# Kernel tuning notes

Hardware: AMD Instinct MI355X
Metric: run time of the kernel (lower is better)

## Reference

```python
import jax, jax.numpy as jnp
import numpy as np

B, LQ, LK, H, A = 32, 2048, 2048, 1024, 512


def setup_inputs() -> dict:
    key = jax.random.key(0)
    ks = jax.random.split(key, 5)
    s = 1.0 / np.sqrt(H)
    return {
        "query": jax.random.normal(ks[0], (B, LQ, H), jnp.float32),
        "key": jax.random.normal(ks[1], (B, LK, H), jnp.float32),
        "Wq": jax.random.normal(ks[2], (H, A), jnp.float32) * s,
        "bq": jnp.zeros((A,), jnp.float32),
        "Wk": jax.random.normal(ks[3], (H, A), jnp.float32) * s,
        "bk": jnp.zeros((A,), jnp.float32),
        "Wv": jax.random.normal(ks[4], (A, 1), jnp.float32) * (1.0 / np.sqrt(A)),
        "bv": jnp.zeros((1,), jnp.float32),
    }


def reference(query, key, Wq, bq, Wk, bk, Wv, bv):
    # Linear projections
    Qp = jnp.einsum("bqh,ha->bqa", query, Wq) + bq          # [B, LQ, A]
    Kp = jnp.einsum("bkh,ha->bka", key, Wk) + bk            # [B, LK, A]
    # Score matrix Q(query) @ K(key)^T
    alpha_mat = jnp.einsum("bqa,bka->bqk", Qp, Kp)          # [B, LQ, LK]
    # Sum over query dim, softmax over key dim
    alpha = jax.nn.softmax(alpha_mat.sum(axis=1, keepdims=True), axis=2)  # [B, 1, LK]
    # Per-key scalar head V applied to projected keys, then weighted combine
    v = jnp.einsum("bka,ao->bko", Kp, Wv) + bv              # [B, LK, 1]
    x = jnp.matmul(alpha, v)[:, 0, :]                        # [B, 1]
    return x
```

## Files before the change

kernel.cpp:

```cpp
#include <hip/hip_runtime.h>
#include <math.h>

#define NB 32
#define LQ 2048
#define LK 2048
#define HD 1024
#define AD 512
#define QCH 32

__global__ void __launch_bounds__(256) k1_qreduce(const float* __restrict__ query,
                                                 const float* __restrict__ Wk,
                                                 const float* __restrict__ Wv,
                                                 const float* __restrict__ bk,
                                                 const float* __restrict__ bv,
                                                 float* __restrict__ partial,
                                                 float* __restrict__ wv_eff,
                                                 float* __restrict__ c_v) {
    int bid = blockIdx.x;
    if (bid < NB * QCH) {
        int b = bid / QCH, qc = bid % QCH;
        int t = threadIdx.x;
        const int QPC = LQ / QCH;
        float4 a0 = {0.f, 0.f, 0.f, 0.f};
        float4 a1 = {0.f, 0.f, 0.f, 0.f};
        const float4* src = (const float4*)(query + ((size_t)b * LQ + (size_t)qc * QPC) * HD);
        for (int q = 0; q < QPC; q += 2) {
            float4 v0 = src[(size_t)q * (HD / 4) + t];
            float4 v1 = src[(size_t)(q + 1) * (HD / 4) + t];
            a0.x += v0.x; a0.y += v0.y; a0.z += v0.z; a0.w += v0.w;
            a1.x += v1.x; a1.y += v1.y; a1.z += v1.z; a1.w += v1.w;
        }
        float4 acc = {a0.x + a1.x, a0.y + a1.y, a0.z + a1.z, a0.w + a1.w};
        float4* dst = (float4*)(partial + ((size_t)qc * NB + b) * HD);
        dst[t] = acc;
    } else if (bid < NB * QCH + 16) {
        int w = threadIdx.x >> 6, lane = threadIdx.x & 63;
        int gw = (bid - NB * QCH) * 4 + w;
        const float4* vv = (const float4*)(Wv);
        for (int r = 0; r < 16; ++r) {
            int h = gw * 16 + r;
            const float4* wr = (const float4*)(Wk + (size_t)h * AD);
            double acc = 0.0;
            #pragma unroll
            for (int j = 0; j < 2; ++j) {
                int f = lane + 64 * j;
                float4 w4 = wr[f];
                float4 v4 = vv[f];
                acc += (double)w4.x * (double)v4.x + (double)w4.y * (double)v4.y
                     + (double)w4.z * (double)v4.z + (double)w4.w * (double)v4.w;
            }
            #pragma unroll
            for (int off = 32; off > 0; off >>= 1) acc += __shfl_down(acc, off);
            if (lane == 0) wv_eff[h] = (float)acc;
        }
    } else {
        if (threadIdx.x < 64) {
            int lane = threadIdx.x;
            const float4* br = (const float4*)(bk);
            const float4* vv = (const float4*)(Wv);
            double acc = 0.0;
            #pragma unroll
            for (int j = 0; j < 2; ++j) {
                int f = lane + 64 * j;
                float4 b4 = br[f];
                float4 v4 = vv[f];
                acc += (double)b4.x * (double)v4.x + (double)b4.y * (double)v4.y
                     + (double)b4.z * (double)v4.z + (double)b4.w * (double)v4.w;
            }
            #pragma unroll
            for (int off = 32; off > 0; off >>= 1) acc += __shfl_down(acc, off);
            if (lane == 0) c_v[0] = (float)(acc + (double)bv[0]);
        }
    }
}

__global__ void __launch_bounds__(256) kB_qsum(const float* __restrict__ partial,
                                               const float* __restrict__ Wq,
                                               const float* __restrict__ bq,
                                               float* __restrict__ qsum) {
    __shared__ float sq[HD];
    __shared__ double red[4][64];
    int b = blockIdx.x >> 3;
    int a0 = (blockIdx.x & 7) * 64;
    int t = threadIdx.x;

    #pragma unroll
    for (int c = 0; c < 4; ++c) {
        int h = t + c * 256;
        float acc = 0.f;
        #pragma unroll 4
        for (int qc = 0; qc < QCH; ++qc)
            acc += partial[((size_t)qc * NB + b) * HD + h];
        sq[h] = acc;
    }
    __syncthreads();

    int w = t >> 6, lane = t & 63;
    int a = a0 + lane;
    const float* wp = Wq + a;
    double c0 = 0.0, c1 = 0.0, c2 = 0.0, c3 = 0.0;
    int hbase = w * 256;
    for (int i = 0; i < 256; i += 4) {
        int h = hbase + i;
        c0 += (double)sq[h]     * (double)wp[(size_t)h * AD];
        c1 += (double)sq[h + 1] * (double)wp[(size_t)(h + 1) * AD];
        c2 += (double)sq[h + 2] * (double)wp[(size_t)(h + 2) * AD];
        c3 += (double)sq[h + 3] * (double)wp[(size_t)(h + 3) * AD];
    }
    red[w][lane] = ((c0 + c1) + (c2 + c3));
    __syncthreads();
    if (t < 64) {
        double s = red[0][t] + red[1][t] + red[2][t] + red[3][t];
        qsum[(size_t)b * AD + a0 + t] = (float)(s + (double)LQ * (double)bq[a0 + t]);
    }
}

__global__ void __launch_bounds__(256) k4_weff(const float* __restrict__ qsum,
                                               const float* __restrict__ Wk,
                                               float* __restrict__ wk_eff) {
    int w = threadIdx.x >> 6, lane = threadIdx.x & 63;
    int widx = blockIdx.x * 4 + w;
    int b = widx >> 10, h = widx & (HD - 1);
    const float4* wr = (const float4*)(Wk + (size_t)h * AD);
    const float4* qs = (const float4*)(qsum + (size_t)b * AD);
    double acc = 0.0;
    #pragma unroll
    for (int j = 0; j < 2; ++j) {
        int f = lane + 64 * j;
        float4 w4 = wr[f];
        float4 q4 = qs[f];
        acc += (double)w4.x * (double)q4.x + (double)w4.y * (double)q4.y
             + (double)w4.z * (double)q4.z + (double)w4.w * (double)q4.w;
    }
    #pragma unroll
    for (int off = 32; off > 0; off >>= 1) acc += __shfl_down(acc, off);
    if (lane == 0) wk_eff[widx] = (float)acc;
}

__global__ void __launch_bounds__(256) k5_scores(const float* __restrict__ key,
                                                 const float* __restrict__ wk_eff,
                                                 const float* __restrict__ wv_eff,
                                                 const float* __restrict__ c_v,
                                                 float* __restrict__ scores,
                                                 float* __restrict__ vvals) {
    __shared__ float lwk[HD];
    __shared__ float lwv[HD];
    int bid = blockIdx.x;
    int b = bid >> 6;
    int k0 = (bid & 63) * 32;
    for (int i = threadIdx.x; i < HD; i += 256) {
        lwk[i] = wk_eff[(size_t)b * HD + i];
        lwv[i] = wv_eff[i];
    }
    __syncthreads();
    int w = threadIdx.x >> 6;
    int lane = threadIdx.x & 63;
    double cv = (double)c_v[0];
    const float4* lwk4 = (const float4*)lwk;
    const float4* lwv4 = (const float4*)lwv;
    for (int r = 0; r < 8; ++r) {
        int k = k0 + w * 8 + r;
        const float4* kr = (const float4*)(key + ((size_t)b * LK + k) * HD);
        double sc = 0.0, vv = 0.0;
        #pragma unroll
        for (int j = 0; j < 4; ++j) {
            int f = lane + 64 * j;
            float4 kv  = kr[f];
            float4 wk4 = lwk4[f];
            float4 wv4 = lwv4[f];
            sc += (double)kv.x * (double)wk4.x + (double)kv.y * (double)wk4.y
                + (double)kv.z * (double)wk4.z + (double)kv.w * (double)wk4.w;
            vv += (double)kv.x * (double)wv4.x + (double)kv.y * (double)wv4.y
                + (double)kv.z * (double)wv4.z + (double)kv.w * (double)wv4.w;
        }
        #pragma unroll
        for (int off = 32; off > 0; off >>= 1) {
            sc += __shfl_down(sc, off);
            vv += __shfl_down(vv, off);
        }
        if (lane == 0) {
            scores[(size_t)b * LK + k] = (float)sc;
            vvals[(size_t)b * LK + k]  = (float)(vv + cv);
        }
    }
}

__global__ void __launch_bounds__(256) k6_softmax(const float* __restrict__ scores,
                                                  const float* __restrict__ vvals,
                                                  float* __restrict__ out) {
    int b = blockIdx.x;
    int t = threadIdx.x;
    __shared__ float smax_sh[4];
    __shared__ double num_sh[4], den_sh[4];
    const float* sr = scores + (size_t)b * LK;
    const float* vr = vvals  + (size_t)b * LK;
    float m = -INFINITY;
    for (int k = t; k < LK; k += 256) m = fmaxf(m, sr[k]);
    #pragma unroll
    for (int off = 32; off > 0; off >>= 1) m = fmaxf(m, __shfl_down(m, off));
    int w = t >> 6, lane = t & 63;
    if (lane == 0) smax_sh[w] = m;
    __syncthreads();
    float gm = fmaxf(fmaxf(smax_sh[0], smax_sh[1]), fmaxf(smax_sh[2], smax_sh[3]));
    double num = 0.0, den = 0.0;
    for (int k = t; k < LK; k += 256) {
        double e = exp((double)(sr[k] - gm));
        den += e;
        num += e * (double)vr[k];
    }
    #pragma unroll
    for (int off = 32; off > 0; off >>= 1) {
        num += __shfl_down(num, off);
        den += __shfl_down(den, off);
    }
    if (lane == 0) { num_sh[w] = num; den_sh[w] = den; }
    __syncthreads();
    if (t == 0) {
        double N = num_sh[0] + num_sh[1] + num_sh[2] + num_sh[3];
        double D = den_sh[0] + den_sh[1] + den_sh[2] + den_sh[3];
        out[b] = (float)(N / D);
    }
}

extern "C" void kernel_launch(void* const* d_in, const int* in_sizes, int n_in,
                              void* d_out, int out_size, void* d_ws, size_t ws_size,
                              hipStream_t stream) {
    const float* query = (const float*)d_in[0];
    const float* key   = (const float*)d_in[1];
    const float* Wq    = (const float*)d_in[2];
    const float* bq    = (const float*)d_in[3];
    const float* Wk    = (const float*)d_in[4];
    const float* bk    = (const float*)d_in[5];
    const float* Wv    = (const float*)d_in[6];
    const float* bv    = (const float*)d_in[7];
    float* out = (float*)d_out;

    float* ws = (float*)d_ws;
    size_t off = 0;
    float* partial = ws + off; off += (size_t)QCH * NB * HD;
    float* qsum    = ws + off; off += (size_t)NB * AD;
    float* wk_eff  = ws + off; off += (size_t)NB * HD;
    float* wv_eff  = ws + off; off += (size_t)HD;
    float* c_v     = ws + off; off += 1;
    float* scores  = ws + off; off += (size_t)NB * LK;
    float* vvals   = ws + off; off += (size_t)NB * LK;

    hipLaunchKernelGGL(k1_qreduce, dim3(NB * QCH + 16 + 1), dim3(256), 0, stream,
                       query, Wk, Wv, bk, bv, partial, wv_eff, c_v);
    hipLaunchKernelGGL(kB_qsum, dim3(NB * 8), dim3(256), 0, stream, partial, Wq, bq, qsum);
    hipLaunchKernelGGL(k4_weff, dim3(NB * HD / 4), dim3(256), 0, stream, qsum, Wk, wk_eff);
    hipLaunchKernelGGL(k5_scores, dim3(NB * (LK / 32)), dim3(256), 0, stream,
                       key, wk_eff, wv_eff, c_v, scores, vvals);
    hipLaunchKernelGGL(k6_softmax, dim3(NB), dim3(256), 0, stream, scores, vvals, out);
}
```

Baseline: 148.6 us.

## Fuse query projection and key-weight reduction into one per-batch kernel

Merges the qsum projection kernel and the effective key-weight kernel into one kernel, launched as a single 512-thread block per batch, so the intermediate qsum no longer goes through global memory and one launch disappears. Also doubles the number of query chunks in the streaming reduction and unrolls it four-wide, and makes the score kernel process two key rows per pass to expose more loads in flight. The price is that the fused stage runs on only 32 blocks. Each block streams all of Wq and Wk serially with double-precision accumulation, which may leave most of the GPU idle.

```diff
diff --git a/kernel.cpp b/kernel.cpp
--- a/kernel.cpp
+++ b/kernel.cpp
@@ -6,37 +6,38 @@
 #define LK 2048
 #define HD 1024
 #define AD 512
-#define QCH 32
-
-__global__ void __launch_bounds__(256) k1_qreduce(const float* __restrict__ query,
-                                                 const float* __restrict__ Wk,
-                                                 const float* __restrict__ Wv,
-                                                 const float* __restrict__ bk,
-                                                 const float* __restrict__ bv,
-                                                 float* __restrict__ partial,
-                                                 float* __restrict__ wv_eff,
-                                                 float* __restrict__ c_v) {
-    int bid = blockIdx.x;
+#define QCH 64
+
+__global__ void __launch_bounds__(256)
+k1_stream(const float* __restrict__ query, const float* __restrict__ Wk,
+          const float* __restrict__ Wv, const float* __restrict__ bk,
+          const float* __restrict__ bv, float* __restrict__ partial,
+          float* __restrict__ wv_eff, float* __restrict__ c_v) {
+    const int bid = blockIdx.x;
+    const int t = threadIdx.x;
     if (bid < NB * QCH) {
         int b = bid / QCH, qc = bid % QCH;
-        int t = threadIdx.x;
         const int QPC = LQ / QCH;
-        float4 a0 = {0.f, 0.f, 0.f, 0.f};
-        float4 a1 = {0.f, 0.f, 0.f, 0.f};
+        float4 a0 = {0.f,0.f,0.f,0.f}, a1 = {0.f,0.f,0.f,0.f};
+        float4 a2 = {0.f,0.f,0.f,0.f}, a3 = {0.f,0.f,0.f,0.f};
         const float4* src = (const float4*)(query + ((size_t)b * LQ + (size_t)qc * QPC) * HD);
-        for (int q = 0; q < QPC; q += 2) {
-            float4 v0 = src[(size_t)q * (HD / 4) + t];
+        for (int q = 0; q < QPC; q += 4) {
+            float4 v0 = src[(size_t)(q + 0) * (HD / 4) + t];
             float4 v1 = src[(size_t)(q + 1) * (HD / 4) + t];
+            float4 v2 = src[(size_t)(q + 2) * (HD / 4) + t];
+            float4 v3 = src[(size_t)(q + 3) * (HD / 4) + t];
             a0.x += v0.x; a0.y += v0.y; a0.z += v0.z; a0.w += v0.w;
             a1.x += v1.x; a1.y += v1.y; a1.z += v1.z; a1.w += v1.w;
-        }
-        float4 acc = {a0.x + a1.x, a0.y + a1.y, a0.z + a1.z, a0.w + a1.w};
-        float4* dst = (float4*)(partial + ((size_t)qc * NB + b) * HD);
-        dst[t] = acc;
+            a2.x += v2.x; a2.y += v2.y; a2.z += v2.z; a2.w += v2.w;
+            a3.x += v3.x; a3.y += v3.y; a3.z += v3.z; a3.w += v3.w;
+        }
+        float4 acc = {(a0.x + a1.x) + (a2.x + a3.x), (a0.y + a1.y) + (a2.y + a3.y),
+                      (a0.z + a1.z) + (a2.z + a3.z), (a0.w + a1.w) + (a2.w + a3.w)};
+        ((float4*)(partial + ((size_t)qc * NB + b) * HD))[t] = acc;
     } else if (bid < NB * QCH + 16) {
-        int w = threadIdx.x >> 6, lane = threadIdx.x & 63;
+        int w = t >> 6, lane = t & 63;
         int gw = (bid - NB * QCH) * 4 + w;
-        const float4* vv = (const float4*)(Wv);
+        const float4* vv = (const float4*)Wv;
         for (int r = 0; r < 16; ++r) {
             int h = gw * 16 + r;
             const float4* wr = (const float4*)(Wk + (size_t)h * AD);
@@ -46,148 +47,154 @@
                 int f = lane + 64 * j;
                 float4 w4 = wr[f];
                 float4 v4 = vv[f];
-                acc += (double)w4.x * (double)v4.x + (double)w4.y * (double)v4.y
-                     + (double)w4.z * (double)v4.z + (double)w4.w * (double)v4.w;
+                acc += (double)w4.x * v4.x + (double)w4.y * v4.y
+                     + (double)w4.z * v4.z + (double)w4.w * v4.w;
             }
             #pragma unroll
             for (int off = 32; off > 0; off >>= 1) acc += __shfl_down(acc, off);
             if (lane == 0) wv_eff[h] = (float)acc;
         }
-    } else {
-        if (threadIdx.x < 64) {
-            int lane = threadIdx.x;
-            const float4* br = (const float4*)(bk);
-            const float4* vv = (const float4*)(Wv);
-            double acc = 0.0;
-            #pragma unroll
-            for (int j = 0; j < 2; ++j) {
-                int f = lane + 64 * j;
-                float4 b4 = br[f];
-                float4 v4 = vv[f];
-                acc += (double)b4.x * (double)v4.x + (double)b4.y * (double)v4.y
-                     + (double)b4.z * (double)v4.z + (double)b4.w * (double)v4.w;
-            }
-            #pragma unroll
-            for (int off = 32; off > 0; off >>= 1) acc += __shfl_down(acc, off);
-            if (lane == 0) c_v[0] = (float)(acc + (double)bv[0]);
-        }
-    }
-}
-
-__global__ void __launch_bounds__(256) kB_qsum(const float* __restrict__ partial,
-                                               const float* __restrict__ Wq,
-                                               const float* __restrict__ bq,
-                                               float* __restrict__ qsum) {
+    } else if (t < 64) {
+        int lane = t;
+        const float4* br = (const float4*)bk;
+        const float4* vv = (const float4*)Wv;
+        double acc = 0.0;
+        #pragma unroll
+        for (int j = 0; j < 2; ++j) {
+            int f = lane + 64 * j;
+            float4 b4 = br[f];
+            float4 v4 = vv[f];
+            acc += (double)b4.x * v4.x + (double)b4.y * v4.y
+                 + (double)b4.z * v4.z + (double)b4.w * v4.w;
+        }
+        #pragma unroll
+        for (int off = 32; off > 0; off >>= 1) acc += __shfl_down(acc, off);
+        if (lane == 0) c_v[0] = (float)(acc + (double)bv[0]);
+    }
+}
+
+__global__ void __launch_bounds__(512)
+k2_qk(const float* __restrict__ partial, const float* __restrict__ Wq,
+      const float* __restrict__ bq, const float* __restrict__ Wk,
+      float* __restrict__ wk_eff) {
     __shared__ float sq[HD];
-    __shared__ double red[4][64];
-    int b = blockIdx.x >> 3;
-    int a0 = (blockIdx.x & 7) * 64;
-    int t = threadIdx.x;
-
-    #pragma unroll
-    for (int c = 0; c < 4; ++c) {
-        int h = t + c * 256;
-        float acc = 0.f;
-        #pragma unroll 4
-        for (int qc = 0; qc < QCH; ++qc)
-            acc += partial[((size_t)qc * NB + b) * HD + h];
-        sq[h] = acc;
+    __shared__ float qs[AD];
+    const int b = blockIdx.x;
+    const int t = threadIdx.x;
+
+    {
+        float ax = 0.f, ay = 0.f;
+        for (int qc = 0; qc < QCH; ++qc) {
+            const float* p = partial + ((size_t)qc * NB + b) * HD + 2 * t;
+            ax += p[0];
+            ay += p[1];
+        }
+        sq[2 * t] = ax;
+        sq[2 * t + 1] = ay;
+    }
+    __syncthreads();
+
+    {
+        int a = t;
+        const float* wp = Wq + a;
+        double c0 = 0.0, c1 = 0.0;
+        for (int h = 0; h < HD; h += 2) {
+            c0 += (double)sq[h]     * wp[(size_t)h * AD];
+            c1 += (double)sq[h + 1] * wp[(size_t)(h + 1) * AD];
+        }
+        qs[a] = (float)(c0 + c1 + (double)LQ * (double)bq[a]);
     }
     __syncthreads();
 
     int w = t >> 6, lane = t & 63;
-    int a = a0 + lane;
-    const float* wp = Wq + a;
-    double c0 = 0.0, c1 = 0.0, c2 = 0.0, c3 = 0.0;
-    int hbase = w * 256;
-    for (int i = 0; i < 256; i += 4) {
-        int h = hbase + i;
-        c0 += (double)sq[h]     * (double)wp[(size_t)h * AD];
-        c1 += (double)sq[h + 1] * (double)wp[(size_t)(h + 1) * AD];
-        c2 += (double)sq[h + 2] * (double)wp[(size_t)(h + 2) * AD];
-        c3 += (double)sq[h + 3] * (double)wp[(size_t)(h + 3) * AD];
-    }
-    red[w][lane] = ((c0 + c1) + (c2 + c3));
-    __syncthreads();
-    if (t < 64) {
-        double s = red[0][t] + red[1][t] + red[2][t] + red[3][t];
-        qsum[(size_t)b * AD + a0 + t] = (float)(s + (double)LQ * (double)bq[a0 + t]);
-    }
-}
-
-__global__ void __launch_bounds__(256) k4_weff(const float* __restrict__ qsum,
-                                               const float* __restrict__ Wk,
-                                               float* __restrict__ wk_eff) {
-    int w = threadIdx.x >> 6, lane = threadIdx.x & 63;
-    int widx = blockIdx.x * 4 + w;
-    int b = widx >> 10, h = widx & (HD - 1);
-    const float4* wr = (const float4*)(Wk + (size_t)h * AD);
-    const float4* qs = (const float4*)(qsum + (size_t)b * AD);
-    double acc = 0.0;
-    #pragma unroll
-    for (int j = 0; j < 2; ++j) {
-        int f = lane + 64 * j;
-        float4 w4 = wr[f];
-        float4 q4 = qs[f];
-        acc += (double)w4.x * (double)q4.x + (double)w4.y * (double)q4.y
-             + (double)w4.z * (double)q4.z + (double)w4.w * (double)q4.w;
-    }
-    #pragma unroll
-    for (int off = 32; off > 0; off >>= 1) acc += __shfl_down(acc, off);
-    if (lane == 0) wk_eff[widx] = (float)acc;
-}
-
-__global__ void __launch_bounds__(256) k5_scores(const float* __restrict__ key,
-                                                 const float* __restrict__ wk_eff,
-                                                 const float* __restrict__ wv_eff,
-                                                 const float* __restrict__ c_v,
-                                                 float* __restrict__ scores,
-                                                 float* __restrict__ vvals) {
+    const float4* qs4 = (const float4*)qs;
+    for (int r = 0; r < 128; r += 2) {
+        int h0 = w * 128 + r;
+        const float4* r0 = (const float4*)(Wk + (size_t)h0 * AD);
+        const float4* r1 = (const float4*)(Wk + (size_t)(h0 + 1) * AD);
+        double a0 = 0.0, a1 = 0.0;
+        #pragma unroll
+        for (int j = 0; j < 2; ++j) {
+            int f = lane + 64 * j;
+            float4 w0 = r0[f];
+            float4 w1 = r1[f];
+            float4 q4 = qs4[f];
+            a0 += (double)w0.x * q4.x + (double)w0.y * q4.y
+                + (double)w0.z * q4.z + (double)w0.w * q4.w;
+            a1 += (double)w1.x * q4.x + (double)w1.y * q4.y
+                + (double)w1.z * q4.z + (double)w1.w * q4.w;
+        }
+        #pragma unroll
+        for (int off = 32; off > 0; off >>= 1) {
+            a0 += __shfl_down(a0, off);
+            a1 += __shfl_down(a1, off);
+        }
+        if (lane == 0) {
+            wk_eff[(size_t)b * HD + h0]     = (float)a0;
+            wk_eff[(size_t)b * HD + h0 + 1] = (float)a1;
+        }
+    }
+}
+
+__global__ void __launch_bounds__(256)
+k3_scores(const float* __restrict__ key, const float* __restrict__ wk_eff,
+          const float* __restrict__ wv_eff, const float* __restrict__ c_v,
+          float* __restrict__ scores, float* __restrict__ vvals) {
     __shared__ float lwk[HD];
     __shared__ float lwv[HD];
-    int bid = blockIdx.x;
-    int b = bid >> 6;
-    int k0 = (bid & 63) * 32;
-    for (int i = threadIdx.x; i < HD; i += 256) {
+    const int bid = blockIdx.x;
+    const int b = bid >> 6;
+    const int k0 = (bid & 63) * 32;
+    const int t = threadIdx.x;
+    for (int i = t; i < HD; i += 256) {
         lwk[i] = wk_eff[(size_t)b * HD + i];
         lwv[i] = wv_eff[i];
     }
     __syncthreads();
-    int w = threadIdx.x >> 6;
-    int lane = threadIdx.x & 63;
+    int w = t >> 6, lane = t & 63;
     double cv = (double)c_v[0];
     const float4* lwk4 = (const float4*)lwk;
     const float4* lwv4 = (const float4*)lwv;
-    for (int r = 0; r < 8; ++r) {
-        int k = k0 + w * 8 + r;
-        const float4* kr = (const float4*)(key + ((size_t)b * LK + k) * HD);
-        double sc = 0.0, vv = 0.0;
+    for (int rp = 0; rp < 4; ++rp) {
+        int k = k0 + w * 8 + rp * 2;
+        const float4* kr0 = (const float4*)(key + ((size_t)b * LK + k) * HD);
+        const float4* kr1 = kr0 + (HD / 4);
+        double sc0 = 0.0, vv0 = 0.0, sc1 = 0.0, vv1 = 0.0;
         #pragma unroll
         for (int j = 0; j < 4; ++j) {
             int f = lane + 64 * j;
-            float4 kv  = kr[f];
+            float4 k0v = kr0[f];
+            float4 k1v = kr1[f];
             float4 wk4 = lwk4[f];
             float4 wv4 = lwv4[f];
-            sc += (double)kv.x * (double)wk4.x + (double)kv.y * (double)wk4.y
-                + (double)kv.z * (double)wk4.z + (double)kv.w * (double)wk4.w;
-            vv += (double)kv.x * (double)wv4.x + (double)kv.y * (double)wv4.y
-                + (double)kv.z * (double)wv4.z + (double)kv.w * (double)wv4.w;
+            sc0 += (double)k0v.x * wk4.x + (double)k0v.y * wk4.y
+                 + (double)k0v.z * wk4.z + (double)k0v.w * wk4.w;
+            vv0 += (double)k0v.x * wv4.x + (double)k0v.y * wv4.y
+                 + (double)k0v.z * wv4.z + (double)k0v.w * wv4.w;
+            sc1 += (double)k1v.x * wk4.x + (double)k1v.y * wk4.y
+                 + (double)k1v.z * wk4.z + (double)k1v.w * wk4.w;
+            vv1 += (double)k1v.x * wv4.x + (double)k1v.y * wv4.y
+                 + (double)k1v.z * wv4.z + (double)k1v.w * wv4.w;
         }
         #pragma unroll
         for (int off = 32; off > 0; off >>= 1) {
-            sc += __shfl_down(sc, off);
-            vv += __shfl_down(vv, off);
+            sc0 += __shfl_down(sc0, off);
+            vv0 += __shfl_down(vv0, off);
+            sc1 += __shfl_down(sc1, off);
+            vv1 += __shfl_down(vv1, off);
         }
         if (lane == 0) {
-            scores[(size_t)b * LK + k] = (float)sc;
-            vvals[(size_t)b * LK + k]  = (float)(vv + cv);
-        }
-    }
-}
-
-__global__ void __launch_bounds__(256) k6_softmax(const float* __restrict__ scores,
-                                                  const float* __restrict__ vvals,
-                                                  float* __restrict__ out) {
+            scores[(size_t)b * LK + k]     = (float)sc0;
+            vvals [(size_t)b * LK + k]     = (float)(vv0 + cv);
+            scores[(size_t)b * LK + k + 1] = (float)sc1;
+            vvals [(size_t)b * LK + k + 1] = (float)(vv1 + cv);
+        }
+    }
+}
+
+__global__ void __launch_bounds__(256)
+k4_softmax(const float* __restrict__ scores, const float* __restrict__ vvals,
+           float* __restrict__ out) {
     int b = blockIdx.x;
     int t = threadIdx.x;
     __shared__ float smax_sh[4];
@@ -238,18 +245,18 @@
     float* ws = (float*)d_ws;
     size_t off = 0;
     float* partial = ws + off; off += (size_t)QCH * NB * HD;
-    float* qsum    = ws + off; off += (size_t)NB * AD;
     float* wk_eff  = ws + off; off += (size_t)NB * HD;
     float* wv_eff  = ws + off; off += (size_t)HD;
     float* c_v     = ws + off; off += 1;
     float* scores  = ws + off; off += (size_t)NB * LK;
     float* vvals   = ws + off; off += (size_t)NB * LK;
 
-    hipLaunchKernelGGL(k1_qreduce, dim3(NB * QCH + 16 + 1), dim3(256), 0, stream,
+    hipLaunchKernelGGL(k1_stream, dim3(NB * QCH + 16 + 1), dim3(256), 0, stream,
                        query, Wk, Wv, bk, bv, partial, wv_eff, c_v);
-    hipLaunchKernelGGL(kB_qsum, dim3(NB * 8), dim3(256), 0, stream, partial, Wq, bq, qsum);
-    hipLaunchKernelGGL(k4_weff, dim3(NB * HD / 4), dim3(256), 0, stream, qsum, Wk, wk_eff);
-    hipLaunchKernelGGL(k5_scores, dim3(NB * (LK / 32)), dim3(256), 0, stream,
+    hipLaunchKernelGGL(k2_qk, dim3(NB), dim3(512), 0, stream,
+                       partial, Wq, bq, Wk, wk_eff);
+    hipLaunchKernelGGL(k3_scores, dim3(NB * (LK / 32)), dim3(256), 0, stream,
                        key, wk_eff, wv_eff, c_v, scores, vvals);
-    hipLaunchKernelGGL(k6_softmax, dim3(NB), dim3(256), 0, stream, scores, vvals, out);
-}
+    hipLaunchKernelGGL(k4_softmax, dim3(NB), dim3(256), 0, stream,
+                       scores, vvals, out);
+}
```

Result: slower. 211.3 us (+42.2%).
